# Kernel tuning notes

Hardware: AMD Instinct MI355X
Metric: run time of the kernel (lower is better)

Reference implementation:

```python
import jax, jax.numpy as jnp
import numpy as np

DECAY = 0.25
THRESHOLD = 1.0
TIME_STEPS = 20

@jax.custom_vjp
def spike(v):
    return (v > 0).astype(v.dtype)

def _spike_fwd(v):
    return (v > 0).astype(v.dtype), v

def _spike_bwd(v, g):
    return (g / (1.0 + jnp.abs(v)) ** 2,)

spike.defvjp(_spike_fwd, _spike_bwd)


def setup_inputs() -> dict:
    key = jax.random.key(0)
    k_x, k_w1, k_b1, k_w2, k_b2 = jax.random.split(key, 5)
    B = 32768
    x = jax.random.normal(k_x, (B, 784), dtype=jnp.float32)
    # nn.Linear-style init scales
    W1 = jax.random.normal(k_w1, (128, 784), dtype=jnp.float32) / np.sqrt(784)
    b1 = jax.random.normal(k_b1, (128,), dtype=jnp.float32) / np.sqrt(784)
    W2 = jax.random.normal(k_w2, (10, 128), dtype=jnp.float32) / np.sqrt(128)
    b2 = jax.random.normal(k_b2, (10,), dtype=jnp.float32) / np.sqrt(128)
    return {"x": x, "W1": W1, "b1": b1, "W2": W2, "b2": b2}


def reference(x, W1, b1, W2, b2):
    B = x.shape[0]
    # Input current is constant across timesteps; compute the first GEMM once.
    cur1 = x @ W1.T + b1  # [B, 128]

    def step(carry, _):
        mem1, mem2 = carry
        mem1 = mem1 * DECAY + cur1
        spk1 = spike(mem1 - THRESHOLD)
        mem1 = mem1 * (1.0 - spk1)
        mem2 = mem2 * DECAY + spk1 @ W2.T + b2
        spk2 = spike(mem2 - THRESHOLD)
        mem2 = mem2 * (1.0 - spk2)
        return (mem1, mem2), (spk1, spk2)

    init = (jnp.zeros((B, 128), x.dtype), jnp.zeros((B, 10), x.dtype))
    _, (spk1_rec, spk2_rec) = jax.lax.scan(step, init, None, length=TIME_STEPS)
    output = spk2_rec.sum(axis=0)  # [B, 10]
    return output, spk1_rec  # spk1_rec: [T, B, 128]
```

## Files before the change

kernel.cpp:

```cpp
#include <hip/hip_runtime.h>
#include <cstddef>


typedef float f32x4 __attribute__((ext_vector_type(4)));

constexpr int BROWS  = 64;
constexpr int BK     = 16;
constexpr int NJ     = 128;
constexpr int KDIM   = 784;
constexpr int NO     = 10;
constexpr int TSTEPS = 20;

__global__ __launch_bounds__(256, 2) void snn_fused(
    const float* __restrict__ x,
    const float* __restrict__ W1,
    const float* __restrict__ b1,
    const float* __restrict__ W2,
    const float* __restrict__ b2,
    float* __restrict__ out,
    int B)
{
    __shared__ alignas(16) float xs[2][BK][68];
    __shared__ alignas(16) float ws[2][BK][192];
    __shared__ alignas(16) float4 w2s[NJ][3];
    __shared__ unsigned smaskW[2][BROWS][17];
    __shared__ float b2s[12];

    const int t  = threadIdx.x;
    const int tx = t & 15;
    const int ty = t >> 4;
    const int r0 = blockIdx.x * BROWS;

    for (int e = t; e < NJ * 3; e += 256) {
        int og = e % 3, j = e / 3;
        float sc = __int_as_float((127 - (j & 31)) << 23);
        float vv[4];
        #pragma unroll
        for (int c = 0; c < 4; ++c) {
            int o = og * 4 + c;
            vv[c] = (o < NO) ? W2[o * NJ + j] * sc : 0.0f;
        }
        float4 v; v.x = vv[0]; v.y = vv[1]; v.z = vv[2]; v.w = vv[3];
        w2s[j][og] = v;
    }
    if (t < 12) b2s[t] = (t < NO) ? b2[t] : 0.0f;

    float acc[4][8], cur[4][8];
    #pragma unroll
    for (int rr = 0; rr < 4; ++rr)
        #pragma unroll
        for (int jj = 0; jj < 8; ++jj) { acc[rr][jj] = 0.0f; cur[rr][jj] = 0.0f; }

    const int xrow = t >> 2, xkf = (t & 3) * 4;
    const int wj   = t >> 1, wkf = (t & 1) * 8;
    const int wco  = wj >> 3, wci = wj & 7;
    const float* xrp = x  + (size_t)(r0 + xrow) * KDIM + xkf;
    const float* wrp = W1 + (size_t)wj * KDIM + wkf;

    float4 xv = *(const float4*)(xrp);
    float4 wa = *(const float4*)(wrp);
    float4 wb = *(const float4*)(wrp + 4);
    {
        xs[0][xkf + 0][xrow] = xv.x; xs[0][xkf + 1][xrow] = xv.y;
        xs[0][xkf + 2][xrow] = xv.z; xs[0][xkf + 3][xrow] = xv.w;
        float* wp0 = &ws[0][wkf][wco * 12 + wci];
        wp0[0]    = wa.x; wp0[192]  = wa.y; wp0[384]  = wa.z; wp0[576]  = wa.w;
        wp0[768]  = wb.x; wp0[960]  = wb.y; wp0[1152] = wb.z; wp0[1344] = wb.w;
    }
    __syncthreads();

    #pragma unroll 1
    for (int tt = 0; tt < 49; ++tt) {
        const int cb = tt & 1;
        if (tt < 48) {
            const int k0n = (tt + 1) * BK;
            xv = *(const float4*)(xrp + k0n);
            wa = *(const float4*)(wrp + k0n);
            wb = *(const float4*)(wrp + k0n + 4);
        }
        #pragma unroll
        for (int kk = 0; kk < BK; ++kk) {
            float4 xr  = *(const float4*)&xs[cb][kk][ty * 4];
            float4 wva = *(const float4*)&ws[cb][kk][tx * 12];
            float4 wvb = *(const float4*)&ws[cb][kk][tx * 12 + 4];
            float xf[4] = {xr.x, xr.y, xr.z, xr.w};
            float wf[8] = {wva.x, wva.y, wva.z, wva.w, wvb.x, wvb.y, wvb.z, wvb.w};
            #pragma unroll
            for (int rr = 0; rr < 4; ++rr)
                #pragma unroll
                for (int jj = 0; jj < 8; ++jj)
                    acc[rr][jj] = fmaf(xf[rr], wf[jj], acc[rr][jj]);
        }
        if (tt == 19) {
            #pragma unroll
            for (int rr = 0; rr < 4; ++rr)
                #pragma unroll
                for (int jj = 0; jj < 8; ++jj) { cur[rr][jj] = acc[rr][jj]; acc[rr][jj] = 0.0f; }
        } else if (tt == 39) {
            #pragma unroll
            for (int rr = 0; rr < 4; ++rr)
                #pragma unroll
                for (int jj = 0; jj < 8; ++jj) { cur[rr][jj] = cur[rr][jj] + acc[rr][jj]; acc[rr][jj] = 0.0f; }
        }
        if (tt < 48) {
            const int nb = cb ^ 1;
            xs[nb][xkf + 0][xrow] = xv.x; xs[nb][xkf + 1][xrow] = xv.y;
            xs[nb][xkf + 2][xrow] = xv.z; xs[nb][xkf + 3][xrow] = xv.w;
            float* wp0 = &ws[nb][wkf][wco * 12 + wci];
            wp0[0]    = wa.x; wp0[192]  = wa.y; wp0[384]  = wa.z; wp0[576]  = wa.w;
            wp0[768]  = wb.x; wp0[960]  = wb.y; wp0[1152] = wb.z; wp0[1344] = wb.w;
        }
        __syncthreads();
    }
    {
        const float* b1p = b1 + tx * 8;
        float4 ba = *(const float4*)b1p, bb = *(const float4*)(b1p + 4);
        float bf[8] = {ba.x, ba.y, ba.z, ba.w, bb.x, bb.y, bb.z, bb.w};
        #pragma unroll
        for (int rr = 0; rr < 4; ++rr)
            #pragma unroll
            for (int jj = 0; jj < 8; ++jj)
                cur[rr][jj] = (cur[rr][jj] + acc[rr][jj]) + bf[jj];
    }

    float mem1[4][8];
    #pragma unroll
    for (int rr = 0; rr < 4; ++rr)
        #pragma unroll
        for (int jj = 0; jj < 8; ++jj) mem1[rr][jj] = 0.0f;

    const int row_l2 = t & 63;
    const int og     = t >> 6;
    float m2[4]  = {0.f, 0.f, 0.f, 0.f};
    float cnt[4] = {0.f, 0.f, 0.f, 0.f};
    float* rec = out + (size_t)B * NO;

    #pragma unroll 1
    for (int st = 0; st < TSTEPS; ++st) {
        const int p = st & 1;
        #pragma unroll
        for (int rr = 0; rr < 4; ++rr) {
            unsigned bt = 0;
            float s0[8];
            #pragma unroll
            for (int jj = 0; jj < 8; ++jj) {
                float m = fmaf(mem1[rr][jj], 0.25f, cur[rr][jj]);
                float v = m - 1.0f;
                bool  s = v > 0.0f;
                s0[jj] = s ? 1.0f : 0.0f;
                mem1[rr][jj] = s ? 0.0f : m;
                bt |= s ? (1u << jj) : 0u;
            }
            size_t base = ((size_t)st * B + (size_t)(r0 + ty * 4 + rr)) * NJ + tx * 8;
            f32x4 fa = {s0[0], s0[1], s0[2], s0[3]};
            f32x4 fb = {s0[4], s0[5], s0[6], s0[7]};
            __builtin_nontemporal_store(fa, (f32x4*)&rec[base]);
            __builtin_nontemporal_store(fb, (f32x4*)&rec[base + 4]);
            ((unsigned char*)&smaskW[p][ty * 4 + rr][0])[tx] = (unsigned char)bt;
        }
        asm volatile("s_waitcnt lgkmcnt(0)\n\ts_barrier" ::: "memory");
        if (og < 3) {
            unsigned mw[4];
            #pragma unroll
            for (int w = 0; w < 4; ++w) mw[w] = smaskW[p][row_l2][w];
            float mm[4] = {0.f, 0.f, 0.f, 0.f};
            #pragma unroll
            for (int w = 0; w < 4; ++w) {
                unsigned bits = mw[w];
                #pragma unroll
                for (int b = 0; b < 32; ++b) {
                    float f = (float)(bits & (1u << b));
                    float4 wv = w2s[w * 32 + b][og];
                    mm[0] = fmaf(f, wv.x, mm[0]);
                    mm[1] = fmaf(f, wv.y, mm[1]);
                    mm[2] = fmaf(f, wv.z, mm[2]);
                    mm[3] = fmaf(f, wv.w, mm[3]);
                }
            }
            #pragma unroll
            for (int c = 0; c < 4; ++c) {
                float cur2 = mm[c] + b2s[og * 4 + c];
                float nm   = fmaf(m2[c], 0.25f, cur2);
                float v2   = nm - 1.0f;
                bool  s2   = v2 > 0.0f;
                cnt[c] += s2 ? 1.0f : 0.0f;
                m2[c]  = s2 ? 0.0f : nm;
            }
        }
    }

    if (og < 3) {
        #pragma unroll
        for (int c = 0; c < 4; ++c) {
            int o = og * 4 + c;
            if (o < NO) out[(size_t)(r0 + row_l2) * NO + o] = cnt[c];
        }
    }
}

extern "C" void kernel_launch(void* const* d_in, const int* in_sizes, int n_in,
                              void* d_out, int out_size, void* d_ws, size_t ws_size,
                              hipStream_t stream)
{
    const float* x  = (const float*)d_in[0];
    const float* W1 = (const float*)d_in[1];
    const float* b1 = (const float*)d_in[2];
    const float* W2 = (const float*)d_in[3];
    const float* b2 = (const float*)d_in[4];
    float* out = (float*)d_out;
    const int B = in_sizes[0] / KDIM;
    snn_fused<<<B / BROWS, 256, 0, stream>>>(x, W1, b1, W2, b2, out, B);
}
```

Baseline: 500.0 us.

## Exchange spike masks via wavefront shuffles instead of LDS and block barrier

```diff
diff --git a/kernel.cpp b/kernel.cpp
--- a/kernel.cpp
+++ b/kernel.cpp
@@ -22,17 +22,15 @@
 {
     __shared__ alignas(16) float xs[2][BK][68];
     __shared__ alignas(16) float ws[2][BK][192];
-    __shared__ alignas(16) float4 w2s[NJ][3];
-    __shared__ unsigned smaskW[2][BROWS][17];
-    __shared__ float b2s[12];
+    __shared__ alignas(16) float4 w2s4[NJ][4];
 
     const int t  = threadIdx.x;
     const int tx = t & 15;
     const int ty = t >> 4;
     const int r0 = blockIdx.x * BROWS;
 
-    for (int e = t; e < NJ * 3; e += 256) {
-        int og = e % 3, j = e / 3;
+    for (int e = t; e < NJ * 4; e += 256) {
+        int og = e & 3, j = e >> 2;
         float sc = __int_as_float((127 - (j & 31)) << 23);
         float vv[4];
         #pragma unroll
@@ -41,9 +39,8 @@
             vv[c] = (o < NO) ? W2[o * NJ + j] * sc : 0.0f;
         }
         float4 v; v.x = vv[0]; v.y = vv[1]; v.z = vv[2]; v.w = vv[3];
-        w2s[j][og] = v;
-    }
-    if (t < 12) b2s[t] = (t < NO) ? b2[t] : 0.0f;
+        w2s4[j][og] = v;
+    }
 
     float acc[4][8], cur[4][8];
     #pragma unroll
@@ -129,15 +126,28 @@
         #pragma unroll
         for (int jj = 0; jj < 8; ++jj) mem1[rr][jj] = 0.0f;
 
-    const int row_l2 = t & 63;
-    const int og     = t >> 6;
+    const int l    = t & 63;
+    const int og   = l & 3;
+    const int rl   = l >> 2;
+    const int wv   = t >> 6;
+    const int grow = wv * 16 + rl;
+    const int srcb = (l >> 4) << 4;
+    const int shb  = (l & 12) << 1;
+    float b2r[4] = {0.f, 0.f, 0.f, 0.f};
+    if (og < 3) {
+        #pragma unroll
+        for (int c = 0; c < 4; ++c) {
+            int o = og * 4 + c;
+            b2r[c] = (o < NO) ? b2[o] : 0.0f;
+        }
+    }
     float m2[4]  = {0.f, 0.f, 0.f, 0.f};
     float cnt[4] = {0.f, 0.f, 0.f, 0.f};
     float* rec = out + (size_t)B * NO;
 
     #pragma unroll 1
     for (int st = 0; st < TSTEPS; ++st) {
-        const int p = st & 1;
+        unsigned word = 0;
         #pragma unroll
         for (int rr = 0; rr < 4; ++rr) {
             unsigned bt = 0;
@@ -156,13 +166,20 @@
             f32x4 fb = {s0[4], s0[5], s0[6], s0[7]};
             __builtin_nontemporal_store(fa, (f32x4*)&rec[base]);
             __builtin_nontemporal_store(fb, (f32x4*)&rec[base + 4]);
-            ((unsigned char*)&smaskW[p][ty * 4 + rr][0])[tx] = (unsigned char)bt;
-        }
-        asm volatile("s_waitcnt lgkmcnt(0)\n\ts_barrier" ::: "memory");
-        if (og < 3) {
-            unsigned mw[4];
-            #pragma unroll
-            for (int w = 0; w < 4; ++w) mw[w] = smaskW[p][row_l2][w];
+            word |= bt << (8 * rr);
+        }
+        unsigned mw[4];
+        #pragma unroll
+        for (int w = 0; w < 4; ++w) {
+            unsigned m = 0;
+            #pragma unroll
+            for (int k = 0; k < 4; ++k) {
+                unsigned v = (unsigned)__shfl((int)word, srcb + w * 4 + k);
+                m |= ((v >> shb) & 0xFFu) << (8 * k);
+            }
+            mw[w] = m;
+        }
+        {
             float mm[4] = {0.f, 0.f, 0.f, 0.f};
             #pragma unroll
             for (int w = 0; w < 4; ++w) {
@@ -170,16 +187,16 @@
                 #pragma unroll
                 for (int b = 0; b < 32; ++b) {
                     float f = (float)(bits & (1u << b));
-                    float4 wv = w2s[w * 32 + b][og];
-                    mm[0] = fmaf(f, wv.x, mm[0]);
-                    mm[1] = fmaf(f, wv.y, mm[1]);
-                    mm[2] = fmaf(f, wv.z, mm[2]);
-                    mm[3] = fmaf(f, wv.w, mm[3]);
+                    float4 wv2 = w2s4[w * 32 + b][og];
+                    mm[0] = fmaf(f, wv2.x, mm[0]);
+                    mm[1] = fmaf(f, wv2.y, mm[1]);
+                    mm[2] = fmaf(f, wv2.z, mm[2]);
+                    mm[3] = fmaf(f, wv2.w, mm[3]);
                 }
             }
             #pragma unroll
             for (int c = 0; c < 4; ++c) {
-                float cur2 = mm[c] + b2s[og * 4 + c];
+                float cur2 = mm[c] + b2r[c];
                 float nm   = fmaf(m2[c], 0.25f, cur2);
                 float v2   = nm - 1.0f;
                 bool  s2   = v2 > 0.0f;
@@ -193,7 +210,7 @@
         #pragma unroll
         for (int c = 0; c < 4; ++c) {
             int o = og * 4 + c;
-            if (o < NO) out[(size_t)(r0 + row_l2) * NO + o] = cnt[c];
+            if (o < NO) out[(size_t)(r0 + grow) * NO + o] = cnt[c];
         }
     }
 }
```

After: 1.227 ms. +145.5%, slower.
